# Kernel optimization log

Measured on AMD Instinct MI355X. Metric: run time of the kernel, lower is better.

Reference implementation:

```python
import jax, jax.numpy as jnp
import numpy as np

B, C = 1024, 256
GRID_H, GRID_W, PAD_H, PAD_W = 11, 15, 13, 17  # 165 hexes, padded 13x17

def _build_convinds():
    off0 = np.array([-17, -16, -1, 0, 1, 17, 18])
    off1 = np.array([-18, -17, -1, 0, 1, 16, 17])
    inds = np.zeros((GRID_H, GRID_W, 7), dtype=np.int32)
    for y in range(1, GRID_H + 1):
        for x in range(1, GRID_W + 1):
            off = off0 if y % 2 == 0 else off1
            inds[y - 1, x - 1] = off + (y * PAD_W + x)
    return jnp.asarray(inds.reshape(-1))  # (165*7,)

CONVINDS = _build_convinds()

def hexconv(x, W, b):
    # x: (B, 165, C); W: (7C, C); b: (C,)
    bsz = x.shape[0]
    c = x.shape[-1]
    padded = jnp.zeros((bsz, PAD_H, PAD_W, c), x.dtype)
    padded = padded.at[:, 1:1 + GRID_H, 1:1 + GRID_W, :].set(x.reshape(bsz, GRID_H, GRID_W, c))
    padded = padded.reshape(bsz, PAD_H * PAD_W, c)
    gathered = padded[:, CONVINDS, :].reshape(bsz, GRID_H * GRID_W, 7 * c)  # (B,165,7C)
    return gathered @ W + b

def leaky(v):
    return jax.nn.leaky_relu(v, negative_slope=0.01)

def setup_inputs() -> dict:
    key = jax.random.key(0)
    k1, k2, k3, k4, k5 = jax.random.split(key, 5)
    scale = 1.0 / np.sqrt(7 * C)
    return {
        "x": jax.random.normal(k1, (B, 165, C), dtype=jnp.float32),
        "W1": jax.random.uniform(k2, (7 * C, C), jnp.float32, -scale, scale),
        "b1": jax.random.uniform(k3, (C,), jnp.float32, -scale, scale),
        "W2": jax.random.uniform(k4, (7 * C, C), jnp.float32, -scale, scale),
        "b2": jax.random.uniform(k5, (C,), jnp.float32, -scale, scale),
    }

def reference(x, W1, b1, W2, b2):
    # depth=1 residual block: x = act(conv2(act(conv1(x))) + x)
    h = leaky(hexconv(x, W1, b1))
    return leaky(hexconv(h, W2, b2) + x)
```

## Files before the change

kernel.cpp:

```cpp
#include <hip/hip_runtime.h>

typedef __attribute__((ext_vector_type(8))) short short8;
typedef __attribute__((ext_vector_type(4))) float f32x4;

typedef __attribute__((address_space(1))) const unsigned int guint;
typedef __attribute__((address_space(3))) unsigned int luint;

__device__ __forceinline__ void gload16(const void* g, void* l) {
    __builtin_amdgcn_global_load_lds((guint*)g, (luint*)l, 16, 0, 0);
}

__device__ __forceinline__ unsigned short f2bf(float f) {
    unsigned u = __float_as_uint(f);
    u += 0x7fffu + ((u >> 16) & 1u);
    return (unsigned short)(u >> 16);
}
__device__ __forceinline__ float bf2f(unsigned short s) {
    return __uint_as_float((unsigned)s << 16);
}

__device__ const int g_DY[7]  = {-1, -1, 0, 0, 0, 1, 1};
__device__ const int g_DXO[7] = { 0,  1, -1, 0, 1, 0, 1};
__device__ const int g_DXE[7] = {-1,  0, -1, 0, 1, -1, 0};

__global__ void __launch_bounds__(256) cvt_x_kernel(const float* __restrict__ in,
                                                    unsigned short* __restrict__ out,
                                                    int n8) {
    int stride = gridDim.x * blockDim.x;
    for (int i = blockIdx.x * blockDim.x + threadIdx.x; i < n8; i += stride) {
        const float4* p = reinterpret_cast<const float4*>(in) + (size_t)i * 2;
        float4 a = p[0], b = p[1];
        short8 o;
        o[0] = (short)f2bf(a.x); o[1] = (short)f2bf(a.y);
        o[2] = (short)f2bf(a.z); o[3] = (short)f2bf(a.w);
        o[4] = (short)f2bf(b.x); o[5] = (short)f2bf(b.y);
        o[6] = (short)f2bf(b.z); o[7] = (short)f2bf(b.w);
        *reinterpret_cast<short8*>(out + (size_t)i * 8) = o;
    }
}

__global__ void __launch_bounds__(256) cvt_wt_kernel(const float* __restrict__ W1,
                                                     const float* __restrict__ W2,
                                                     unsigned short* __restrict__ W1t,
                                                     unsigned short* __restrict__ W2t) {
    const float* W = blockIdx.z ? W2 : W1;
    unsigned short* Wt = blockIdx.z ? W2t : W1t;
    int k0 = blockIdx.x * 64;
    int n0 = blockIdx.y * 64;
    __shared__ float tile[64][65];
    for (int e = threadIdx.x; e < 4096; e += 256) {
        int r = e >> 6, c = e & 63;
        tile[r][c] = W[(size_t)(k0 + r) * 256 + n0 + c];
    }
    __syncthreads();
    for (int e = threadIdx.x; e < 4096; e += 256) {
        int r = e >> 6, c = e & 63;
        Wt[(size_t)(n0 + r) * 1792 + k0 + c] = f2bf(tile[c][r]);
    }
}

template <int MODE>
__global__ void __launch_bounds__(512, 2) hexconv8_kernel(
        const unsigned short* __restrict__ xg,
        const unsigned short* __restrict__ wt,
        const float* __restrict__ bias,
        const unsigned short* __restrict__ residbf,
        void* __restrict__ outp,
        const unsigned short* __restrict__ zp)
{
    __shared__ unsigned short smem[65536];

    const int t = threadIdx.x;
    const int lane = t & 63, w = t >> 6;
    const int wr = w >> 2, wc = w & 3;

    int bid = blockIdx.x;
    int xcd = bid & 7, idx = bid >> 3;
    const int mb = (xcd < 4 ? xcd * 83 : 332 + (xcd - 4) * 82) + idx;

    const int trow = t >> 3;
    const int chunk = t & 7;
    const int aswz = (chunk ^ (trow & 7)) * 8;
    int yv[4], xv[4], brow[4], aoff[4];
    const unsigned short* wsrcp[4];
#pragma unroll
    for (int i = 0; i < 4; ++i) {
        int row = i * 64 + trow;
        int m = mb * 256 + row;
        int b = m / 165;
        int ii = m - b * 165;
        int y = ii / 15;
        int x = ii - y * 15;
        yv[i] = y; xv[i] = x; brow[i] = m - ii;
        wsrcp[i] = wt + (size_t)row * 1792 + aswz;
    }

#define CALC_AOFF(J) do {                                                     \
        int dy_ = g_DY[J];                                                    \
        int dxo_ = g_DXO[J], dxe_ = g_DXE[J];                                 \
        _Pragma("unroll")                                                     \
        for (int i = 0; i < 4; ++i) {                                         \
            int dx_ = (yv[i] & 1) ? dxo_ : dxe_;                              \
            int ny_ = yv[i] + dy_, nx_ = xv[i] + dx_;                         \
            bool v_ = ((unsigned)ny_ < 11u) && ((unsigned)nx_ < 15u);         \
            aoff[i] = v_ ? ((brow[i] + ny_ * 15 + nx_) * 256 + aswz) : -1;    \
        } } while (0)

    int offA[4][2], offB[2][2][2];
    {
        int l15 = lane & 15, lhi = lane >> 4, l7 = lane & 7;
#pragma unroll
        for (int f = 0; f < 4; ++f)
#pragma unroll
            for (int ks = 0; ks < 2; ++ks)
                offA[f][ks] = (wr * 128 + f * 16 + l15) * 64 + (((ks * 4 + lhi) ^ l7) * 8);
#pragma unroll
        for (int nh = 0; nh < 2; ++nh)
#pragma unroll
            for (int g = 0; g < 2; ++g)
#pragma unroll
                for (int ks = 0; ks < 2; ++ks)
                    offB[nh][g][ks] = (wc * 64 + nh * 32 + g * 16 + l15) * 64 +
                                      (((ks * 4 + lhi) ^ l7) * 8);
    }

    f32x4 acc[8][4];
#pragma unroll
    for (int mf = 0; mf < 8; ++mf)
#pragma unroll
        for (int nf = 0; nf < 4; ++nf) {
            f32x4 z = {0.f, 0.f, 0.f, 0.f};
            acc[mf][nf] = z;
        }
    short8 a[4][2], b0[2][2], b1[2][2];

#define STAGE_A_ONE(I, TT, Q) do { int c0_ = ((TT) & 3) * 64;                 \
        const unsigned short* g_ = (aoff[I] >= 0) ? (xg + aoff[I] + c0_) : zp; \
        gload16(g_, &smem[(Q) * 32768 + (I) * 4096 + t * 8]); } while (0)
#define STAGE_B_ALL(TT, Q) do { int ko_ = (TT) * 64;                          \
        _Pragma("unroll")                                                     \
        for (int i = 0; i < 4; ++i)                                           \
            gload16(wsrcp[i] + ko_, &smem[(Q) * 32768 + 16384 + i * 4096 + t * 8]); \
        } while (0)

#define LDA(P, MH) do { _Pragma("unroll") for (int f = 0; f < 4; ++f)         \
        _Pragma("unroll") for (int ks = 0; ks < 2; ++ks)                      \
            a[f][ks] = *(const short8*)&smem[(P) * 32768 + (MH) * 4096 + offA[f][ks]]; \
        } while (0)
#define LDB(P, NH, DST) do { _Pragma("unroll") for (int g = 0; g < 2; ++g)    \
        _Pragma("unroll") for (int ks = 0; ks < 2; ++ks)                      \
            DST[g][ks] = *(const short8*)&smem[(P) * 32768 + 16384 + offB[NH][g][ks]]; \
        } while (0)

#define QUAD(MH, NH, BF) do { _Pragma("unroll") for (int f = 0; f < 4; ++f)   \
        _Pragma("unroll") for (int g = 0; g < 2; ++g)                         \
        _Pragma("unroll") for (int ks = 0; ks < 2; ++ks)                      \
            acc[(MH) * 4 + f][(NH) * 2 + g] = __builtin_amdgcn_mfma_f32_16x16x32_bf16( \
                a[f][ks], BF[g][ks], acc[(MH) * 4 + f][(NH) * 2 + g], 0, 0, 0); \
        } while (0)

#define BAR() __builtin_amdgcn_s_barrier()
#define LGKM0() do { asm volatile("s_waitcnt lgkmcnt(0)" ::: "memory");       \
                     __builtin_amdgcn_sched_barrier(0); } while (0)
#define VMCNT(N) do { asm volatile("s_waitcnt vmcnt(" #N ")" ::: "memory");   \
                      __builtin_amdgcn_sched_barrier(0); } while (0)
#define PRIO(N) __builtin_amdgcn_s_setprio(N)

#define TILE(T28, P) do {                                                     \
        int tt_ = (T28) + 1;                                                  \
        bool st_ = (tt_ < 28);                                                \
                          \
        if (st_) {                                                            \
            if ((tt_ & 3) == 0) CALC_AOFF(tt_ >> 2);                          \
            STAGE_B_ALL(tt_, 1 - (P));                                        \
            STAGE_A_ONE(0, tt_, 1 - (P));                                     \
            STAGE_A_ONE(2, tt_, 1 - (P));                                     \
        }                                                                     \
        LDA(P, 0); LDB(P, 0, b0);                                             \
        BAR(); LGKM0(); PRIO(1); QUAD(0, 0, b0); PRIO(0); BAR();              \
                                   \
        if (st_) {                                                            \
            STAGE_A_ONE(1, tt_, 1 - (P));                                     \
            STAGE_A_ONE(3, tt_, 1 - (P));                                     \
        }                                                                     \
        LDB(P, 1, b1);                                                        \
        BAR(); LGKM0(); PRIO(1); QUAD(0, 1, b1); PRIO(0);                     \
        if (st_) { VMCNT(8); } else { VMCNT(0); }       \
        BAR();                                                                \
                                                                      \
        LDA(P, 1);                                                            \
        BAR(); LGKM0(); PRIO(1); QUAD(1, 1, b1); PRIO(0); BAR();              \
                                                                      \
        PRIO(1); QUAD(1, 0, b0); PRIO(0);                                     \
        if (st_) { VMCNT(2); } else { VMCNT(0); }       \
        BAR();                                                                \
    } while (0)

    CALC_AOFF(0);
    STAGE_B_ALL(0, 0);
    STAGE_A_ONE(0, 0, 0); STAGE_A_ONE(2, 0, 0);
    STAGE_A_ONE(1, 0, 0); STAGE_A_ONE(3, 0, 0);
    VMCNT(0); BAR();

#pragma unroll 1
    for (int it = 0; it < 14; ++it) {
        TILE(2 * it, 0);
        TILE(2 * it + 1, 1);
    }

    const size_t mrowbase = (size_t)mb * 256 + wr * 128;
    const int l15 = lane & 15, lq = (lane >> 4) * 4;
    if (MODE == 0) {
        unsigned short* outh = (unsigned short*)outp;
#pragma unroll
        for (int nf = 0; nf < 4; ++nf) {
            int col = wc * 64 + nf * 16 + l15;
            float bb = bias[col];
#pragma unroll
            for (int mf = 0; mf < 8; ++mf)
#pragma unroll
                for (int r = 0; r < 4; ++r) {
                    size_t mr = mrowbase + mf * 16 + lq + r;
                    float v = acc[mf][nf][r] + bb;
                    v = v > 0.f ? v : 0.01f * v;
                    outh[mr * 256 + col] = f2bf(v);
                }
        }
    } else {
        float* outf = (float*)outp;
#pragma unroll
        for (int nf = 0; nf < 4; ++nf) {
            int col = wc * 64 + nf * 16 + l15;
            float bb = bias[col];
#pragma unroll
            for (int mf = 0; mf < 8; ++mf)
#pragma unroll
                for (int r = 0; r < 4; ++r) {
                    size_t mr = mrowbase + mf * 16 + lq + r;
                    float v = acc[mf][nf][r] + bb + bf2f(residbf[mr * 256 + col]);
                    v = v > 0.f ? v : 0.01f * v;
                    outf[mr * 256 + col] = v;
                }
        }
    }
}

extern "C" void kernel_launch(void* const* d_in, const int* in_sizes, int n_in,
                              void* d_out, int out_size, void* d_ws, size_t ws_size,
                              hipStream_t stream) {
    const float* x  = (const float*)d_in[0];
    const float* W1 = (const float*)d_in[1];
    const float* b1 = (const float*)d_in[2];
    const float* W2 = (const float*)d_in[3];
    const float* b2 = (const float*)d_in[4];
    float* out = (float*)d_out;

    const size_t XBF = (size_t)1024 * 165 * 256 * 2;
    const size_t WTB = (size_t)256 * 1792 * 2;
    char* ws = (char*)d_ws;
    unsigned short* zp  = (unsigned short*)ws;
    unsigned short* xbf = (unsigned short*)(ws + 256);
    unsigned short* hbf = (unsigned short*)(ws + 256 + XBF);
    unsigned short* w1t = (unsigned short*)(ws + 256 + 2 * XBF);
    unsigned short* w2t = (unsigned short*)(ws + 256 + 2 * XBF + WTB);

    hipMemsetAsync(d_ws, 0, 256, stream);
    cvt_x_kernel<<<2048, 256, 0, stream>>>(x, xbf, 5406720);
    cvt_wt_kernel<<<dim3(28, 4, 2), 256, 0, stream>>>(W1, W2, w1t, w2t);
    hexconv8_kernel<0><<<660, 512, 0, stream>>>(xbf, w1t, b1, nullptr, (void*)hbf, zp);
    hexconv8_kernel<1><<<660, 512, 0, stream>>>(hbf, w2t, b2, xbf, (void*)out, zp);
}
```

Baseline: 458.6 us.

## Merge per-tile barrier phases, encode hex offsets as constants, stage bf16 epilogue through LDS

The main loop tile is restructured so all global-to-LDS staging is issued up front, and the LDS fragment loads for each M-half are batched. Two MFMA quads then run back to back with fewer barriers per tile. Neighbor offsets are now decoded from packed integer constants instead of device-memory tables. The bf16 intermediate output in the first conv is written through a per-wave LDS buffer so global stores are 16-byte vectorized rows. The intent is to cut barrier and sync overhead and scattered 2-byte stores, at the cost of less interleaving between staging and compute.

```diff
diff --git a/kernel.cpp b/kernel.cpp
--- a/kernel.cpp
+++ b/kernel.cpp
@@ -18,10 +18,6 @@
 __device__ __forceinline__ float bf2f(unsigned short s) {
     return __uint_as_float((unsigned)s << 16);
 }
-
-__device__ const int g_DY[7]  = {-1, -1, 0, 0, 0, 1, 1};
-__device__ const int g_DXO[7] = { 0,  1, -1, 0, 1, 0, 1};
-__device__ const int g_DXE[7] = {-1,  0, -1, 0, 1, -1, 0};
 
 __global__ void __launch_bounds__(256) cvt_x_kernel(const float* __restrict__ in,
                                                     unsigned short* __restrict__ out,
@@ -96,8 +92,9 @@
     }
 
 #define CALC_AOFF(J) do {                                                     \
-        int dy_ = g_DY[J];                                                    \
-        int dxo_ = g_DXO[J], dxe_ = g_DXE[J];                                 \
+        int dy_  = ((10576 >> (2 * (J))) & 3) - 1;                            \
+        int dxo_ = ((9801  >> (2 * (J))) & 3) - 1;                            \
+        int dxe_ = ((4676  >> (2 * (J))) & 3) - 1;                            \
         _Pragma("unroll")                                                     \
         for (int i = 0; i < 4; ++i) {                                         \
             int dx_ = (yv[i] & 1) ? dxo_ : dxe_;                              \
@@ -166,32 +163,25 @@
                       __builtin_amdgcn_sched_barrier(0); } while (0)
 #define PRIO(N) __builtin_amdgcn_s_setprio(N)
 
-#define TILE(T28, P) do {                                                     \
+#define TILE2(T28, P) do {                                                    \
         int tt_ = (T28) + 1;                                                  \
         bool st_ = (tt_ < 28);                                                \
-                          \
+                    \
         if (st_) {                                                            \
             if ((tt_ & 3) == 0) CALC_AOFF(tt_ >> 2);                          \
             STAGE_B_ALL(tt_, 1 - (P));                                        \
             STAGE_A_ONE(0, tt_, 1 - (P));                                     \
             STAGE_A_ONE(2, tt_, 1 - (P));                                     \
-        }                                                                     \
-        LDA(P, 0); LDB(P, 0, b0);                                             \
-        BAR(); LGKM0(); PRIO(1); QUAD(0, 0, b0); PRIO(0); BAR();              \
-                                   \
-        if (st_) {                                                            \
             STAGE_A_ONE(1, tt_, 1 - (P));                                     \
             STAGE_A_ONE(3, tt_, 1 - (P));                                     \
         }                                                                     \
-        LDB(P, 1, b1);                                                        \
-        BAR(); LGKM0(); PRIO(1); QUAD(0, 1, b1); PRIO(0);                     \
+        LDA(P, 0); LDB(P, 0, b0); LDB(P, 1, b1);                              \
+        LGKM0(); PRIO(1); QUAD(0, 0, b0); QUAD(0, 1, b1); PRIO(0);            \
         if (st_) { VMCNT(8); } else { VMCNT(0); }       \
         BAR();                                                                \
-                                                                      \
+                                              \
         LDA(P, 1);                                                            \
-        BAR(); LGKM0(); PRIO(1); QUAD(1, 1, b1); PRIO(0); BAR();              \
-                                                                      \
-        PRIO(1); QUAD(1, 0, b0); PRIO(0);                                     \
+        LGKM0(); PRIO(1); QUAD(1, 1, b1); QUAD(1, 0, b0); PRIO(0);            \
         if (st_) { VMCNT(2); } else { VMCNT(0); }       \
         BAR();                                                                \
     } while (0)
@@ -204,14 +194,42 @@
 
 #pragma unroll 1
     for (int it = 0; it < 14; ++it) {
-        TILE(2 * it, 0);
-        TILE(2 * it + 1, 1);
+        TILE2(2 * it, 0);
+        TILE2(2 * it + 1, 1);
     }
 
     const size_t mrowbase = (size_t)mb * 256 + wr * 128;
-    const int l15 = lane & 15, lq = (lane >> 4) * 4;
+    const int l15 = lane & 15, lhi = lane >> 4;
     if (MODE == 0) {
         unsigned short* outh = (unsigned short*)outp;
+        unsigned short* my = smem + w * (64 * 68);
+#pragma unroll 1
+        for (int h = 0; h < 2; ++h) {
+            __syncthreads();
+#pragma unroll
+            for (int mf2 = 0; mf2 < 4; ++mf2) {
+#pragma unroll
+                for (int nf = 0; nf < 4; ++nf) {
+                    float bb = bias[wc * 64 + nf * 16 + l15];
+#pragma unroll
+                    for (int r = 0; r < 4; ++r) {
+                        float v = acc[h * 4 + mf2][nf][r] + bb;
+                        v = v > 0.f ? v : 0.01f * v;
+                        my[(mf2 * 16 + lhi * 4 + r) * 68 + nf * 16 + l15] = f2bf(v);
+                    }
+                }
+            }
+            __syncthreads();
+#pragma unroll
+            for (int rr = 0; rr < 8; ++rr) {
+                int row = rr * 8 + (lane >> 3);
+                short8 vv = *(const short8*)&my[row * 68 + (lane & 7) * 8];
+                size_t gm = mrowbase + h * 64 + row;
+                *(short8*)&outh[gm * 256 + wc * 64 + (lane & 7) * 8] = vv;
+            }
+        }
+    } else {
+        float* outf = (float*)outp;
 #pragma unroll
         for (int nf = 0; nf < 4; ++nf) {
             int col = wc * 64 + nf * 16 + l15;
@@ -220,23 +238,7 @@
             for (int mf = 0; mf < 8; ++mf)
 #pragma unroll
                 for (int r = 0; r < 4; ++r) {
-                    size_t mr = mrowbase + mf * 16 + lq + r;
-                    float v = acc[mf][nf][r] + bb;
-                    v = v > 0.f ? v : 0.01f * v;
-                    outh[mr * 256 + col] = f2bf(v);
-                }
-        }
-    } else {
-        float* outf = (float*)outp;
-#pragma unroll
-        for (int nf = 0; nf < 4; ++nf) {
-            int col = wc * 64 + nf * 16 + l15;
-            float bb = bias[col];
-#pragma unroll
-            for (int mf = 0; mf < 8; ++mf)
-#pragma unroll
-                for (int r = 0; r < 4; ++r) {
-                    size_t mr = mrowbase + mf * 16 + lq + r;
+                    size_t mr = mrowbase + mf * 16 + lhi * 4 + r;
                     float v = acc[mf][nf][r] + bb + bf2f(residbf[mr * 256 + col]);
                     v = v > 0.f ? v : 0.01f * v;
                     outf[mr * 256 + col] = v;
```

New measurement: 500.4 us. +9.1%, slower.

## Shrink hexconv GEMM tile to 128x128 with 256-thread blocks and N split

Applied to the files above, without the earlier changes.

Replaces the 256x256 output tile (8 waves, 512 threads) with a 128x128 tile run by 4 waves, splitting N into two halves across blocks and launching 2640 blocks instead of 660. The LDS footprint is halved, the per-tile pipeline is simplified to two MFMA phases with a full vmcnt(0) wait, and the neighbour offset tables move from device constant memory to bit-packed immediates. This aims for better occupancy and load balance across CUs, at the cost of reloading each A gather twice (once per N half), lower arithmetic intensity per block, and a less overlapped prefetch schedule.

```diff
diff --git a/kernel.cpp b/kernel.cpp
--- a/kernel.cpp
+++ b/kernel.cpp
@@ -18,10 +18,6 @@
 __device__ __forceinline__ float bf2f(unsigned short s) {
     return __uint_as_float((unsigned)s << 16);
 }
-
-__device__ const int g_DY[7]  = {-1, -1, 0, 0, 0, 1, 1};
-__device__ const int g_DXO[7] = { 0,  1, -1, 0, 1, 0, 1};
-__device__ const int g_DXE[7] = {-1,  0, -1, 0, 1, -1, 0};
 
 __global__ void __launch_bounds__(256) cvt_x_kernel(const float* __restrict__ in,
                                                     unsigned short* __restrict__ out,
@@ -60,7 +56,7 @@
 }
 
 template <int MODE>
-__global__ void __launch_bounds__(512, 2) hexconv8_kernel(
+__global__ void __launch_bounds__(256, 2) hexconv2_kernel(
         const unsigned short* __restrict__ xg,
         const unsigned short* __restrict__ wt,
         const float* __restrict__ bias,
@@ -68,15 +64,14 @@
         void* __restrict__ outp,
         const unsigned short* __restrict__ zp)
 {
-    __shared__ unsigned short smem[65536];
+    __shared__ unsigned short smem[32768];
 
     const int t = threadIdx.x;
-    const int lane = t & 63, w = t >> 6;
-    const int wr = w >> 2, wc = w & 3;
+    const int lane = t & 63, wc = t >> 6;
 
     int bid = blockIdx.x;
-    int xcd = bid & 7, idx = bid >> 3;
-    const int mb = (xcd < 4 ? xcd * 83 : 332 + (xcd - 4) * 82) + idx;
+    int gl = (bid & 7) * 330 + (bid >> 3);
+    const int mb = gl >> 1, nb = gl & 1;
 
     const int trow = t >> 3;
     const int chunk = t & 7;
@@ -85,19 +80,20 @@
     const unsigned short* wsrcp[4];
 #pragma unroll
     for (int i = 0; i < 4; ++i) {
-        int row = i * 64 + trow;
-        int m = mb * 256 + row;
+        int row = i * 32 + trow;
+        int m = mb * 128 + row;
         int b = m / 165;
         int ii = m - b * 165;
         int y = ii / 15;
         int x = ii - y * 15;
         yv[i] = y; xv[i] = x; brow[i] = m - ii;
-        wsrcp[i] = wt + (size_t)row * 1792 + aswz;
+        wsrcp[i] = wt + (size_t)(nb * 128 + row) * 1792 + aswz;
     }
 
 #define CALC_AOFF(J) do {                                                     \
-        int dy_ = g_DY[J];                                                    \
-        int dxo_ = g_DXO[J], dxe_ = g_DXE[J];                                 \
+        int dy_  = ((10576 >> (2 * (J))) & 3) - 1;                            \
+        int dxo_ = ((9801  >> (2 * (J))) & 3) - 1;                            \
+        int dxe_ = ((4676  >> (2 * (J))) & 3) - 1;                            \
         _Pragma("unroll")                                                     \
         for (int i = 0; i < 4; ++i) {                                         \
             int dx_ = (yv[i] & 1) ? dxo_ : dxe_;                              \
@@ -106,57 +102,54 @@
             aoff[i] = v_ ? ((brow[i] + ny_ * 15 + nx_) * 256 + aswz) : -1;    \
         } } while (0)
 
-    int offA[4][2], offB[2][2][2];
+    int offA_e[2], offB_e[2];
     {
         int l15 = lane & 15, lhi = lane >> 4, l7 = lane & 7;
 #pragma unroll
-        for (int f = 0; f < 4; ++f)
-#pragma unroll
-            for (int ks = 0; ks < 2; ++ks)
-                offA[f][ks] = (wr * 128 + f * 16 + l15) * 64 + (((ks * 4 + lhi) ^ l7) * 8);
-#pragma unroll
-        for (int nh = 0; nh < 2; ++nh)
-#pragma unroll
-            for (int g = 0; g < 2; ++g)
-#pragma unroll
-                for (int ks = 0; ks < 2; ++ks)
-                    offB[nh][g][ks] = (wc * 64 + nh * 32 + g * 16 + l15) * 64 +
-                                      (((ks * 4 + lhi) ^ l7) * 8);
-    }
-
-    f32x4 acc[8][4];
+        for (int ks = 0; ks < 2; ++ks) {
+            offA_e[ks] = l15 * 64 + (((ks * 4 + lhi) ^ l7) * 8);
+            offB_e[ks] = (wc * 32 + l15) * 64 + (((ks * 4 + lhi) ^ l7) * 8);
+        }
+    }
+
+    f32x4 acc[8][2];
 #pragma unroll
     for (int mf = 0; mf < 8; ++mf)
 #pragma unroll
-        for (int nf = 0; nf < 4; ++nf) {
+        for (int nf = 0; nf < 2; ++nf) {
             f32x4 z = {0.f, 0.f, 0.f, 0.f};
             acc[mf][nf] = z;
         }
-    short8 a[4][2], b0[2][2], b1[2][2];
-
-#define STAGE_A_ONE(I, TT, Q) do { int c0_ = ((TT) & 3) * 64;                 \
-        const unsigned short* g_ = (aoff[I] >= 0) ? (xg + aoff[I] + c0_) : zp; \
-        gload16(g_, &smem[(Q) * 32768 + (I) * 4096 + t * 8]); } while (0)
+    short8 a[4][2], b[2][2];
+
+#define STAGE_A_ALL(TT, Q) do { int c0_ = ((TT) & 3) * 64;                    \
+        _Pragma("unroll")                                                     \
+        for (int i = 0; i < 4; ++i) {                                         \
+            const unsigned short* g_ = (aoff[i] >= 0) ? (xg + aoff[i] + c0_) : zp; \
+            gload16(g_, &smem[(Q) * 16384 + i * 2048 + t * 8]);               \
+        } } while (0)
 #define STAGE_B_ALL(TT, Q) do { int ko_ = (TT) * 64;                          \
         _Pragma("unroll")                                                     \
         for (int i = 0; i < 4; ++i)                                           \
-            gload16(wsrcp[i] + ko_, &smem[(Q) * 32768 + 16384 + i * 4096 + t * 8]); \
+            gload16(wsrcp[i] + ko_, &smem[(Q) * 16384 + 8192 + i * 2048 + t * 8]); \
         } while (0)
 
 #define LDA(P, MH) do { _Pragma("unroll") for (int f = 0; f < 4; ++f)         \
         _Pragma("unroll") for (int ks = 0; ks < 2; ++ks)                      \
-            a[f][ks] = *(const short8*)&smem[(P) * 32768 + (MH) * 4096 + offA[f][ks]]; \
-        } while (0)
-#define LDB(P, NH, DST) do { _Pragma("unroll") for (int g = 0; g < 2; ++g)    \
+            a[f][ks] = *(const short8*)&smem[(P) * 16384 + (MH) * 4096 +      \
+                                             f * 1024 + offA_e[ks]];          \
+        } while (0)
+#define LDB(P) do { _Pragma("unroll") for (int g = 0; g < 2; ++g)             \
         _Pragma("unroll") for (int ks = 0; ks < 2; ++ks)                      \
-            DST[g][ks] = *(const short8*)&smem[(P) * 32768 + 16384 + offB[NH][g][ks]]; \
-        } while (0)
-
-#define QUAD(MH, NH, BF) do { _Pragma("unroll") for (int f = 0; f < 4; ++f)   \
+            b[g][ks] = *(const short8*)&smem[(P) * 16384 + 8192 +             \
+                                             g * 1024 + offB_e[ks]];          \
+        } while (0)
+
+#define QUAD(MH) do { _Pragma("unroll") for (int f = 0; f < 4; ++f)           \
         _Pragma("unroll") for (int g = 0; g < 2; ++g)                         \
         _Pragma("unroll") for (int ks = 0; ks < 2; ++ks)                      \
-            acc[(MH) * 4 + f][(NH) * 2 + g] = __builtin_amdgcn_mfma_f32_16x16x32_bf16( \
-                a[f][ks], BF[g][ks], acc[(MH) * 4 + f][(NH) * 2 + g], 0, 0, 0); \
+            acc[(MH) * 4 + f][g] = __builtin_amdgcn_mfma_f32_16x16x32_bf16(   \
+                a[f][ks], b[g][ks], acc[(MH) * 4 + f][g], 0, 0, 0);           \
         } while (0)
 
 #define BAR() __builtin_amdgcn_s_barrier()
@@ -169,37 +162,23 @@
 #define TILE(T28, P) do {                                                     \
         int tt_ = (T28) + 1;                                                  \
         bool st_ = (tt_ < 28);                                                \
-                          \
+                                           \
         if (st_) {                                                            \
             if ((tt_ & 3) == 0) CALC_AOFF(tt_ >> 2);                          \
-            STAGE_B_ALL(tt_, 1 - (P));                                        \
-            STAGE_A_ONE(0, tt_, 1 - (P));                                     \
-            STAGE_A_ONE(2, tt_, 1 - (P));                                     \
+            STAGE_A_ALL(tt_, 1 - (P));                                        \
         }                                                                     \
-        LDA(P, 0); LDB(P, 0, b0);                                             \
-        BAR(); LGKM0(); PRIO(1); QUAD(0, 0, b0); PRIO(0); BAR();              \
-                                   \
-        if (st_) {                                                            \
-            STAGE_A_ONE(1, tt_, 1 - (P));                                     \
-            STAGE_A_ONE(3, tt_, 1 - (P));                                     \
-        }                                                                     \
-        LDB(P, 1, b1);                                                        \
-        BAR(); LGKM0(); PRIO(1); QUAD(0, 1, b1); PRIO(0);                     \
-        if (st_) { VMCNT(8); } else { VMCNT(0); }       \
-        BAR();                                                                \
-                                                                      \
+        LDA(P, 0); LDB(P);                                                    \
+        BAR(); LGKM0(); PRIO(1); QUAD(0); PRIO(0); BAR();                     \
+                                           \
+        if (st_) STAGE_B_ALL(tt_, 1 - (P));                                   \
         LDA(P, 1);                                                            \
-        BAR(); LGKM0(); PRIO(1); QUAD(1, 1, b1); PRIO(0); BAR();              \
-                                                                      \
-        PRIO(1); QUAD(1, 0, b0); PRIO(0);                                     \
-        if (st_) { VMCNT(2); } else { VMCNT(0); }       \
-        BAR();                                                                \
+        BAR(); LGKM0(); PRIO(1); QUAD(1); PRIO(0);                            \
+        VMCNT(0); BAR();                                                      \
     } while (0)
 
     CALC_AOFF(0);
+    STAGE_A_ALL(0, 0);
     STAGE_B_ALL(0, 0);
-    STAGE_A_ONE(0, 0, 0); STAGE_A_ONE(2, 0, 0);
-    STAGE_A_ONE(1, 0, 0); STAGE_A_ONE(3, 0, 0);
     VMCNT(0); BAR();
 
 #pragma unroll 1
@@ -208,13 +187,13 @@
         TILE(2 * it + 1, 1);
     }
 
-    const size_t mrowbase = (size_t)mb * 256 + wr * 128;
+    const size_t mrowbase = (size_t)mb * 128;
     const int l15 = lane & 15, lq = (lane >> 4) * 4;
     if (MODE == 0) {
         unsigned short* outh = (unsigned short*)outp;
 #pragma unroll
-        for (int nf = 0; nf < 4; ++nf) {
-            int col = wc * 64 + nf * 16 + l15;
+        for (int nf = 0; nf < 2; ++nf) {
+            int col = nb * 128 + wc * 32 + nf * 16 + l15;
             float bb = bias[col];
 #pragma unroll
             for (int mf = 0; mf < 8; ++mf)
@@ -229,8 +208,8 @@
     } else {
         float* outf = (float*)outp;
 #pragma unroll
-        for (int nf = 0; nf < 4; ++nf) {
-            int col = wc * 64 + nf * 16 + l15;
+        for (int nf = 0; nf < 2; ++nf) {
+            int col = nb * 128 + wc * 32 + nf * 16 + l15;
             float bb = bias[col];
 #pragma unroll
             for (int mf = 0; mf < 8; ++mf)
@@ -267,6 +246,6 @@
     hipMemsetAsync(d_ws, 0, 256, stream);
     cvt_x_kernel<<<2048, 256, 0, stream>>>(x, xbf, 5406720);
     cvt_wt_kernel<<<dim3(28, 4, 2), 256, 0, stream>>>(W1, W2, w1t, w2t);
-    hexconv8_kernel<0><<<660, 512, 0, stream>>>(xbf, w1t, b1, nullptr, (void*)hbf, zp);
-    hexconv8_kernel<1><<<660, 512, 0, stream>>>(hbf, w2t, b2, xbf, (void*)out, zp);
-}
+    hexconv2_kernel<0><<<2640, 256, 0, stream>>>(xbf, w1t, b1, nullptr, (void*)hbf, zp);
+    hexconv2_kernel<1><<<2640, 256, 0, stream>>>(hbf, w2t, b2, xbf, (void*)out, zp);
+}
```

After: 453.9 us. No clear change (-1.0%).
